# Optimization experiments

Hardware: AMD Instinct MI355X
Metric: run time of the kernel (lower is better)

The kernel has to match this reference:

```python
import jax, jax.numpy as jnp
import numpy as np

WD, WH, WW = 6, 6, 6
NUM_HEADS = 8
EPS = 1e-5


def setup_inputs() -> dict:
    key = jax.random.key(0)
    ks = jax.random.split(key, 4)
    B, C, D, H, W = 1, 128, 48, 48, 48
    return {
        "q_map": jax.random.normal(ks[0], (B, C, D, H, W), dtype=jnp.float32),
        "k_map": jax.random.normal(ks[1], (B, C, D, H, W), dtype=jnp.float32),
        "v_map": jax.random.normal(ks[2], (B, C, D, H, W), dtype=jnp.float32),
        "gamma_q": jnp.ones((C,), jnp.float32),
        "beta_q": jnp.zeros((C,), jnp.float32),
        "gamma_kv": jnp.ones((C,), jnp.float32),
        "beta_kv": jnp.zeros((C,), jnp.float32),
        "proj_w": jax.random.normal(ks[3], (C, C), dtype=jnp.float32) * (1.0 / np.sqrt(C)),
        "proj_b": jnp.zeros((C,), jnp.float32),
    }


def _layernorm(x, g, b):
    m = jnp.mean(x, axis=-1, keepdims=True)
    v = jnp.mean(jnp.square(x - m), axis=-1, keepdims=True)
    return (x - m) * jax.lax.rsqrt(v + EPS) * g + b


def _window_partition(x):
    # x: (B, D, H, W, C) -> windows: (B*nD*nH*nW, wd*wh*ww, C)
    B, D, H, W, C = x.shape
    pd, ph, pw = (WD - D % WD) % WD, (WH - H % WH) % WH, (WW - W % WW) % WW
    if pd or ph or pw:
        x = jnp.pad(x, ((0, 0), (0, pd), (0, ph), (0, pw), (0, 0)))
    Dp, Hp, Wp = D + pd, H + ph, W + pw
    x = x.reshape(B, Dp // WD, WD, Hp // WH, WH, Wp // WW, WW, C)
    x = jnp.transpose(x, (0, 1, 3, 5, 2, 4, 6, 7))
    return x.reshape(-1, WD * WH * WW, C), (D, H, W, Dp, Hp, Wp)


def _window_reverse(windows, meta):
    D, H, W, Dp, Hp, Wp = meta
    C = windows.shape[-1]
    nD, nH, nW = Dp // WD, Hp // WH, Wp // WW
    B = windows.shape[0] // (nD * nH * nW)
    x = windows.reshape(B, nD, nH, nW, WD, WH, WW, C)
    x = jnp.transpose(x, (0, 1, 4, 2, 5, 3, 6, 7)).reshape(B, Dp, Hp, Wp, C)
    return x[:, :D, :H, :W, :]


def reference(q_map, k_map, v_map, gamma_q, beta_q, gamma_kv, beta_kv, proj_w, proj_b):
    # (B, C, D, H, W) -> (B, D, H, W, C)
    q_map = jnp.transpose(q_map, (0, 2, 3, 4, 1))
    k_map = jnp.transpose(k_map, (0, 2, 3, 4, 1))
    v_map = jnp.transpose(v_map, (0, 2, 3, 4, 1))

    q, meta = _window_partition(q_map)
    k, _ = _window_partition(k_map)
    v, _ = _window_partition(v_map)

    q = _layernorm(q, gamma_q, beta_q)
    k = _layernorm(k, gamma_kv, beta_kv)
    v = _layernorm(v, gamma_kv, beta_kv)

    Bw, Nq, C = q.shape
    dh = C // NUM_HEADS
    q = q.reshape(Bw, Nq, NUM_HEADS, dh)
    k = k.reshape(Bw, -1, NUM_HEADS, dh)
    v = v.reshape(Bw, -1, NUM_HEADS, dh)

    scale = 1.0 / np.sqrt(dh).astype(np.float32)
    scores = jnp.einsum("bqhd,bkhd->bhqk", q, k) * scale  # (Bw, h, Nq, Nk)
    attn = jax.nn.softmax(scores, axis=-1)
    out = jnp.einsum("bhqk,bkhd->bqhd", attn, v).reshape(Bw, Nq, C)

    out = out @ proj_w.T + proj_b
    out = _window_reverse(out, meta)
    return jnp.transpose(out, (0, 4, 1, 2, 3))  # (B, C, D, H, W)
```

## Files before the change

kernel.cpp:

```cpp
#include <hip/hip_runtime.h>
#include <hip/hip_bf16.h>

typedef short s16x8 __attribute__((ext_vector_type(8)));
typedef float f32x2 __attribute__((ext_vector_type(2)));
typedef float f32x4 __attribute__((ext_vector_type(4)));
typedef float f32x16 __attribute__((ext_vector_type(16)));
typedef unsigned int u32;
typedef unsigned short u16;
typedef u32 u32x4v __attribute__((ext_vector_type(4)));

#define TOK 216
#define T1 448
#define T2 896
#define SP 110592
#define BUF0 0
#define VOFF 57344
#define WOFF 122880
#define GBOFF 155648
#define LDS_OLD 157696
#define LDS_NEW 155648
#define TENB 28311552ull
#define WSNEED (3ull*TENB + 32768ull)
#define QSCALE 0.360673760f

__device__ __forceinline__ u32 pack2(float a, float b) {
  u16 lo = __builtin_bit_cast(u16, __float2bfloat16(a));
  u16 hi = __builtin_bit_cast(u16, __float2bfloat16(b));
  return (u32)lo | ((u32)hi << 16);
}
__device__ __forceinline__ int swz(int row, int inner) {
  return inner ^ ((row & 7) << 4);
}
__device__ __forceinline__ void gload16(const void* g, void* l) {
  __builtin_amdgcn_global_load_lds(
      (const __attribute__((address_space(1))) void*)g,
      (__attribute__((address_space(3))) void*)l, 16, 0, 0);
}

__device__ __forceinline__ void ln_stats(const f32x2* xv, float& mA, float& rA,
                                         float& mB, float& rB) {
  float sA = 0.f, s2A = 0.f, sB = 0.f, s2B = 0.f;
#pragma unroll
  for (int c = 0; c < 32; ++c) {
    sA += xv[c].x; s2A += xv[c].x * xv[c].x;
    sB += xv[c].y; s2B += xv[c].y * xv[c].y;
  }
  sA += __shfl_xor(sA, 1); s2A += __shfl_xor(s2A, 1);
  sB += __shfl_xor(sB, 1); s2B += __shfl_xor(s2B, 1);
  sA += __shfl_xor(sA, 2); s2A += __shfl_xor(s2A, 2);
  sB += __shfl_xor(sB, 2); s2B += __shfl_xor(s2B, 2);
  mA = sA * (1.0f / 128.0f);
  rA = rsqrtf(s2A * (1.0f / 128.0f) - mA * mA + 1e-5f);
  mB = sB * (1.0f / 128.0f);
  rB = rsqrtf(s2B * (1.0f / 128.0f) - mB * mB + 1e-5f);
}

template<bool MASK>
__device__ __forceinline__ void attn_step(const char* smem, int h, int kt,
                                          s16x8 qfh, int lane,
                                          f32x16& acc, float& lsum) {
  const int half = lane >> 5;
  const int krow = kt * 32 + (lane & 31);
  s16x8 kf = *(const s16x8*)(smem + BUF0 + krow * 256 +
                             swz(krow, h * 32 + half * 16));
  __builtin_amdgcn_s_setprio(1);
  f32x16 st = __builtin_amdgcn_mfma_f32_32x32x16_bf16(kf, qfh, (f32x16){}, 0, 0, 0);
  __builtin_amdgcn_s_setprio(0);
  const int vrow = h * 16 + (lane & 15);
  s16x8 vf0 = *(const s16x8*)(smem + VOFF + vrow * 512 +
                              swz(vrow, kt * 64 + half * 16));
  s16x8 vf1 = *(const s16x8*)(smem + VOFF + vrow * 512 +
                              swz(vrow, kt * 64 + 32 + half * 16));
  const int NR = MASK ? 12 : 16;
  u32 A[8];
  float ts0 = 0.f, ts1 = 0.f;
#pragma unroll
  for (int i = 0; i < 8; ++i) {
    float p0 = (2 * i < NR) ? __builtin_amdgcn_exp2f(st[2 * i]) : 0.f;
    float p1 = (2 * i + 1 < NR) ? __builtin_amdgcn_exp2f(st[2 * i + 1]) : 0.f;
    if (i & 1) ts1 += p0 + p1; else ts0 += p0 + p1;
    A[i] = pack2(p0, p1);
  }
  lsum += ts0 + ts1;
  s16x8 pf0 = __builtin_bit_cast(s16x8, (u32x4v){A[0], A[1], A[2], A[3]});
  s16x8 pf1 = __builtin_bit_cast(s16x8, (u32x4v){A[4], A[5], A[6], A[7]});
  __builtin_amdgcn_s_setprio(1);
  acc = __builtin_amdgcn_mfma_f32_32x32x16_bf16(vf0, pf0, acc, 0, 0, 0);
  acc = __builtin_amdgcn_mfma_f32_32x32x16_bf16(vf1, pf1, acc, 0, 0, 0);
  __builtin_amdgcn_s_setprio(0);
}

extern "C" __global__ __launch_bounds__(256)
void lnpre_kernel(const float* __restrict__ qm, const float* __restrict__ km,
                  const float* __restrict__ vm,
                  const float* __restrict__ gq, const float* __restrict__ bq,
                  const float* __restrict__ gkv, const float* __restrict__ bkv,
                  const float* __restrict__ pw,
                  u16* __restrict__ qn, u16* __restrict__ kn,
                  u16* __restrict__ vn, u16* __restrict__ wbf) {
  const int tid = threadIdx.x;
  const int bid = blockIdx.x;
  if (bid >= 2304) {
#pragma unroll
    for (int k = 0; k < 32; ++k) {
      int idx = tid + 256 * k;
      f32x2 w2 = *(const f32x2*)(pw + idx * 2);
      ((u32*)wbf)[idx] = pack2(w2.x, w2.y);
    }
    return;
  }
  __shared__ float lf[6144];
  __shared__ float gb[512];
  const int d = bid / 48, h = bid - d * 48;
  const int dh = d * 2304 + h * 48;
  if (tid < 128) {
    gb[tid] = gq[tid]; gb[128 + tid] = bq[tid];
    gb[256 + tid] = gkv[tid]; gb[384 + tid] = bkv[tid];
  }
  const int w = tid >> 2, q = tid & 3;
#pragma unroll 1
  for (int t = 0; t < 3; ++t) {
    const float* src = t == 0 ? qm : (t == 1 ? km : vm);
    u16* dst = t == 0 ? qn : (t == 1 ? kn : vn);
    const float* g = (t == 0) ? gb : gb + 256;
    const float* b = (t == 0) ? gb + 128 : gb + 384;
    const float scale = (t == 0) ? QSCALE : 1.0f;
#pragma unroll
    for (int k = 0; k < 6; ++k) {
      int j = tid + 256 * k;
      int ch = j / 12, wq = j - ch * 12;
      *(f32x4*)(lf + ch * 48 + wq * 4) =
          *(const f32x4*)(src + (long)ch * SP + dh + wq * 4);
    }
    __syncthreads();
    if (tid < 192) {
      float s = 0.f, s2 = 0.f;
#pragma unroll
      for (int c = 0; c < 32; ++c) {
        float x = lf[(q + 4 * c) * 48 + w];
        s += x; s2 += x * x;
      }
      s += __shfl_xor(s, 1); s2 += __shfl_xor(s2, 1);
      s += __shfl_xor(s, 2); s2 += __shfl_xor(s2, 2);
      float m = s * (1.f / 128.f);
      float r = rsqrtf(s2 * (1.f / 128.f) - m * m + 1e-5f);
      u32x4v* op = (u32x4v*)(dst + (long)(dh + w) * 128 + 32 * q);
#pragma unroll
      for (int v4 = 0; v4 < 4; ++v4) {
        u32x4v pk;
#pragma unroll
        for (int e = 0; e < 4; ++e) {
          int ch = 32 * q + v4 * 8 + 2 * e;
          float y0 = ((lf[ch * 48 + w] - m) * r * g[ch] + b[ch]) * scale;
          float y1 = ((lf[(ch + 1) * 48 + w] - m) * r * g[ch + 1] + b[ch + 1]) * scale;
          pk[e] = pack2(y0, y1);
        }
        op[v4] = pk;
      }
    }
    __syncthreads();
  }
}

extern "C" __global__ __launch_bounds__(T2, 1)
void attn2_kernel(const u16* __restrict__ qn, const u16* __restrict__ kn,
                  const u16* __restrict__ vn, const u16* __restrict__ wbf,
                  const float* __restrict__ pb, float* __restrict__ out) {
  extern __shared__ __align__(16) char smem[];
  const int tid = threadIdx.x;
  const int lane = tid & 63;
  const int wv = tid >> 6;
  const int wq = wv % 7;
  const int hb = (wv / 7) * 4;
  const int bid = blockIdx.x;
  const int wid = ((bid & 7) << 6) | (bid >> 3);
  const int wd = wid >> 6, wh = (wid >> 3) & 7, ww = wid & 7;
  const int wd6 = wd * 6, wh6 = wh * 6, ww6 = ww * 6;
  const int boff = wd6 * 2304 + wh6 * 48 + ww6;

  for (int uu = wv; uu < 140; uu += 14) {
    const u16* s; char* d;
    if (uu < 54) {
      int u = uu, row = 4 * u + (lane >> 4);
      int tq = row / 6;
      int g = (wd6 + tq / 6) * 2304 + (wh6 + tq % 6) * 48 + ww6 + row % 6;
      s = qn + g * 128 + (((lane & 15) ^ (row & 7)) << 3);
      d = smem + BUF0 + u * 1024;
    } else if (uu < 108) {
      int u = uu - 54, row = 4 * u + (lane >> 4);
      int tq = row / 6;
      int g = (wd6 + tq / 6) * 2304 + (wh6 + tq % 6) * 48 + ww6 + row % 6;
      s = vn + g * 128 + ((lane & 15) << 3);
      d = smem + VOFF + u * 1024;
    } else {
      int u = uu - 108, row = 4 * u + (lane >> 4);
      s = wbf + row * 128 + (((lane & 15) ^ (row & 7)) << 3);
      d = smem + WOFF + u * 1024;
    }
    gload16(s, d);
  }
  __syncthreads();

  s16x8 qf[4];
  {
    int row = wq * 32 + (lane & 31);
    int ib = (lane >> 5) * 16;
#pragma unroll
    for (int j = 0; j < 4; ++j)
      qf[j] = *(const s16x8*)(smem + BUF0 + row * 256 +
                              swz(row, (hb + j) * 32 + ib));
  }
  __syncthreads();

  for (int uu = wv; uu < 54; uu += 14) {
    int row = 4 * uu + (lane >> 4);
    int tq = row / 6;
    int g = (wd6 + tq / 6) * 2304 + (wh6 + tq % 6) * 48 + ww6 + row % 6;
    gload16(kn + g * 128 + (((lane & 15) ^ (row & 7)) << 3),
            smem + BUF0 + uu * 1024);
  }
  u32 tr[16];
#pragma unroll
  for (int k = 0; k < 8; ++k) {
    int u = tid + 896 * k;
    if (u < 6912) {
      int t = (u >> 6) * 2, c2 = u & 63;
      tr[2 * k]     = *(const u32*)(smem + VOFF + t * 256 + c2 * 4);
      tr[2 * k + 1] = *(const u32*)(smem + VOFF + t * 256 + 256 + c2 * 4);
    }
  }
  __syncthreads();

#pragma unroll
  for (int k = 0; k < 8; ++k) {
    int u = tid + 896 * k;
    if (u < 6912) {
      int t = (u >> 6) * 2, c2 = u & 63;
      int st = (t & ~12) | ((t & 4) << 1) | ((t & 8) >> 1);
      int c = 2 * c2;
      u32 w0 = (tr[2 * k] & 0xFFFFu) | (tr[2 * k + 1] << 16);
      u32 w1 = (tr[2 * k] >> 16) | (tr[2 * k + 1] & 0xFFFF0000u);
      *(u32*)(smem + VOFF + c * 512 + ((st * 2) ^ ((c & 7) << 4))) = w0;
      *(u32*)(smem + VOFF + (c + 1) * 512 + ((st * 2) ^ (((c + 1) & 7) << 4))) = w1;
    }
  }
  if (tid < 128) {
    int x = (tid & 7) << 4;
    *(u32*)(smem + VOFF + tid * 512 + (424 ^ x)) = 0;
    *(u32*)(smem + VOFF + tid * 512 + (428 ^ x)) = 0;
    *(u32*)(smem + VOFF + tid * 512 + (440 ^ x)) = 0;
    *(u32*)(smem + VOFF + tid * 512 + (444 ^ x)) = 0;
  }
  __syncthreads();

  u32 oPk[4][4];
#pragma unroll
  for (int hp = 0; hp < 2; ++hp) {
    const int h0 = hb + 2 * hp, h1 = h0 + 1;
    f32x16 a0 = {}, a1 = {};
    float l0 = 0.f, l1 = 0.f;
#pragma unroll 2
    for (int kt = 0; kt < 6; ++kt) {
      attn_step<false>(smem, h0, kt, qf[2 * hp], lane, a0, l0);
      attn_step<false>(smem, h1, kt, qf[2 * hp + 1], lane, a1, l1);
    }
    attn_step<true>(smem, h0, 6, qf[2 * hp], lane, a0, l0);
    attn_step<true>(smem, h1, 6, qf[2 * hp + 1], lane, a1, l1);
    l0 += __shfl_xor(l0, 32);
    l1 += __shfl_xor(l1, 32);
    float i0 = 1.0f / l0, i1 = 1.0f / l1;
#pragma unroll
    for (int r = 0; r < 4; ++r) {
      oPk[2 * hp][r]     = pack2(a0[2 * r] * i0, a0[2 * r + 1] * i0);
      oPk[2 * hp + 1][r] = pack2(a1[2 * r] * i1, a1[2 * r + 1] * i1);
    }
  }
  __syncthreads();

  {
    const int tok = wq * 32 + (lane & 31);
    const int half = lane >> 5;
#pragma unroll
    for (int j = 0; j < 4; ++j) {
      int chb = (hb + j) * 32 + half * 8;
      *(u32*)(smem + BUF0 + tok * 256 + swz(tok, chb))      = oPk[j][0];
      *(u32*)(smem + BUF0 + tok * 256 + swz(tok, chb + 4))  = oPk[j][1];
      *(u32*)(smem + BUF0 + tok * 256 + swz(tok, chb + 16)) = oPk[j][2];
      *(u32*)(smem + BUF0 + tok * 256 + swz(tok, chb + 20)) = oPk[j][3];
    }
  }
  __syncthreads();

  {
    int tok = wv * 16 + (lane & 15);
    s16x8 bfr[4];
#pragma unroll
    for (int kk = 0; kk < 4; ++kk)
      bfr[kk] = *(const s16x8*)(smem + BUF0 + tok * 256 +
                                swz(tok, kk * 64 + (lane >> 4) * 16));
    bool tokValid = tok < TOK;
    int tdd = tok / 36, trr = tok - tdd * 36;
    int thh = trr / 6, tww = trr - thh * 6;
    int pos = boff + tdd * 2304 + thh * 48 + tww;
#pragma unroll 1
    for (int jt = 0; jt < 8; ++jt) {
      f32x4 acc = {};
#pragma unroll
      for (int kk = 0; kk < 4; ++kk) {
        int rw = jt * 16 + (lane & 15);
        s16x8 af = *(const s16x8*)(smem + WOFF + rw * 256 +
                                   swz(rw, kk * 64 + (lane >> 4) * 16));
        acc = __builtin_amdgcn_mfma_f32_16x16x32_bf16(af, bfr[kk], acc, 0, 0, 0);
      }
      f32x4 pbv = *(const f32x4*)(pb + jt * 16 + (lane >> 4) * 4);
      if (tokValid) {
#pragma unroll
        for (int r = 0; r < 4; ++r) {
          int j = jt * 16 + (lane >> 4) * 4 + r;
          out[j * SP + pos] = acc[r] + pbv[r];
        }
      }
    }
  }
}

extern "C" __global__ __launch_bounds__(T1, 2)
void ca3d_kernel(const float* __restrict__ qm, const float* __restrict__ km,
                 const float* __restrict__ vm,
                 const float* __restrict__ gq, const float* __restrict__ bq,
                 const float* __restrict__ gkv, const float* __restrict__ bkv,
                 const float* __restrict__ pw, const float* __restrict__ pb,
                 float* __restrict__ out) {
  extern __shared__ __align__(16) char smem[];
  const int tid = threadIdx.x;
  const int lane = tid & 63;
  const int wv = tid >> 6;
  const int bid = blockIdx.x;
  const int wid = ((bid & 7) << 6) | (bid >> 3);
  const int wd = wid >> 6, wh = (wid >> 3) & 7, ww = wid & 7;
  const int boff = wd * 6 * 2304 + wh * 6 * 48 + ww * 6;

  for (int i = tid * 16; i < VOFF + 65536; i += T1 * 16)
    *(f32x4*)(smem + i) = (f32x4){};
  if (tid < 128) {
    ((float*)(smem + GBOFF))[tid] = gq[tid];
    ((float*)(smem + GBOFF + 512))[tid] = bq[tid];
    ((float*)(smem + GBOFF + 1024))[tid] = gkv[tid];
    ((float*)(smem + GBOFF + 1536))[tid] = bkv[tid];
  }
  const bool lnAct = tid < 432;
  const int tp = tid >> 2;
  const int cbase = (tid & 3) * 32;
  const int tA = tp * 2, tB = tA + 1;
  int td = tA / 36, tr_ = tA - td * 36;
  int th_ = tr_ / 6, tw_ = tr_ - th_ * 6;
  const int gpos = boff + td * 2304 + th_ * 48 + tw_;
  const int vposA = (tA & ~0xC) | ((tA & 4) << 1) | ((tA & 8) >> 1);

  f32x2 qv[32], kv[32], vv[32];
  if (lnAct) {
#pragma unroll
    for (int c = 0; c < 32; ++c)
      qv[c] = *(const f32x2*)(qm + gpos + (cbase + c) * SP);
#pragma unroll
    for (int c = 0; c < 32; ++c)
      kv[c] = *(const f32x2*)(km + gpos + (cbase + c) * SP);
  }
  __syncthreads();
  const float* gql = (const float*)(smem + GBOFF);
  const float* bql = (const float*)(smem + GBOFF + 512);
  const float* gkl = (const float*)(smem + GBOFF + 1024);
  const float* bkl = (const float*)(smem + GBOFF + 1536);
  if (lnAct) {
    float mA, rA, mB, rB;
    ln_stats(qv, mA, rA, mB, rB);
#pragma unroll
    for (int c = 0; c < 32; c += 2) {
      int cc = cbase + c;
      float g0 = gql[cc], g1 = gql[cc + 1], b0 = bql[cc], b1 = bql[cc + 1];
      *(u32*)(smem + BUF0 + tA * 256 + swz(tA, cc * 2)) =
          pack2(((qv[c].x - mA) * rA * g0 + b0) * QSCALE,
                ((qv[c + 1].x - mA) * rA * g1 + b1) * QSCALE);
      *(u32*)(smem + BUF0 + tB * 256 + swz(tB, cc * 2)) =
          pack2(((qv[c].y - mB) * rB * g0 + b0) * QSCALE,
                ((qv[c + 1].y - mB) * rB * g1 + b1) * QSCALE);
    }
#pragma unroll
    for (int c = 0; c < 32; ++c)
      vv[c] = *(const f32x2*)(vm + gpos + (cbase + c) * SP);
  }
  __syncthreads();
  s16x8 qf[8];
  {
    int row = wv * 32 + (lane & 31);
    int ib = (lane >> 5) * 16;
#pragma unroll
    for (int h = 0; h < 8; ++h)
      qf[h] = *(const s16x8*)(smem + BUF0 + row * 256 + swz(row, h * 32 + ib));
  }
  __syncthreads();
  if (lnAct) {
    {
      float mA, rA, mB, rB;
      ln_stats(kv, mA, rA, mB, rB);
#pragma unroll
      for (int c = 0; c < 32; c += 2) {
        int cc = cbase + c;
        float g0 = gkl[cc], g1 = gkl[cc + 1], b0 = bkl[cc], b1 = bkl[cc + 1];
        *(u32*)(smem + BUF0 + tA * 256 + swz(tA, cc * 2)) =
            pack2((kv[c].x - mA) * rA * g0 + b0,
                  (kv[c + 1].x - mA) * rA * g1 + b1);
        *(u32*)(smem + BUF0 + tB * 256 + swz(tB, cc * 2)) =
            pack2((kv[c].y - mB) * rB * g0 + b0,
                  (kv[c + 1].y - mB) * rB * g1 + b1);
      }
    }
    {
      float mA, rA, mB, rB;
      ln_stats(vv, mA, rA, mB, rB);
#pragma unroll
      for (int c = 0; c < 32; ++c) {
        int cc = cbase + c;
        float g0 = gkl[cc], b0 = bkl[cc];
        *(u32*)(smem + VOFF + cc * 512 + swz(cc, vposA * 2)) =
            pack2((vv[c].x - mA) * rA * g0 + b0,
                  (vv[c].y - mB) * rB * g0 + b0);
      }
    }
  }
  for (int i = tid; i < 8192; i += T1) {
    int j = i >> 6, c2 = i & 63;
    f32x2 w2 = *(const f32x2*)(pw + j * 128 + c2 * 2);
    *(u32*)(smem + WOFF + j * 256 + swz(j, c2 * 4)) = pack2(w2.x, w2.y);
  }
  __syncthreads();
  u32 oPk[8][4];
#pragma unroll
  for (int hp = 0; hp < 4; ++hp) {
    const int h0 = hp * 2, h1 = h0 + 1;
    f32x16 a0 = {}, a1 = {};
    float l0 = 0.f, l1 = 0.f;
#pragma unroll 1
    for (int kt = 0; kt < 6; ++kt) {
      attn_step<false>(smem, h0, kt, qf[h0], lane, a0, l0);
      attn_step<false>(smem, h1, kt, qf[h1], lane, a1, l1);
    }
    attn_step<true>(smem, h0, 6, qf[h0], lane, a0, l0);
    attn_step<true>(smem, h1, 6, qf[h1], lane, a1, l1);
    l0 += __shfl_xor(l0, 32);
    l1 += __shfl_xor(l1, 32);
    float i0 = 1.0f / l0, i1 = 1.0f / l1;
#pragma unroll
    for (int r = 0; r < 4; ++r) {
      oPk[h0][r] = pack2(a0[2 * r] * i0, a0[2 * r + 1] * i0);
      oPk[h1][r] = pack2(a1[2 * r] * i1, a1[2 * r + 1] * i1);
    }
  }
  __syncthreads();
  {
    const int tok = wv * 32 + (lane & 31);
    const int half = lane >> 5;
#pragma unroll
    for (int h = 0; h < 8; ++h) {
      int chb = h * 32 + half * 8;
      *(u32*)(smem + BUF0 + tok * 256 + swz(tok, chb))      = oPk[h][0];
      *(u32*)(smem + BUF0 + tok * 256 + swz(tok, chb + 4))  = oPk[h][1];
      *(u32*)(smem + BUF0 + tok * 256 + swz(tok, chb + 16)) = oPk[h][2];
      *(u32*)(smem + BUF0 + tok * 256 + swz(tok, chb + 20)) = oPk[h][3];
    }
  }
  __syncthreads();
#pragma unroll 1
  for (int ti = 0; ti < 2; ++ti) {
    int tt = wv * 2 + ti;
    int tok = tt * 16 + (lane & 15);
    s16x8 bfr[4];
#pragma unroll
    for (int kk = 0; kk < 4; ++kk)
      bfr[kk] = *(const s16x8*)(smem + BUF0 + tok * 256 +
                                swz(tok, kk * 64 + (lane >> 4) * 16));
    bool tokValid = tok < TOK;
    int tdd = tok / 36, trr = tok - tdd * 36;
    int thh = trr / 6, tww = trr - thh * 6;
    int pos = boff + tdd * 2304 + thh * 48 + tww;
#pragma unroll 1
    for (int jt = 0; jt < 8; ++jt) {
      f32x4 acc = {};
#pragma unroll
      for (int kk = 0; kk < 4; ++kk) {
        int rw = jt * 16 + (lane & 15);
        s16x8 af = *(const s16x8*)(smem + WOFF + rw * 256 +
                                   swz(rw, kk * 64 + (lane >> 4) * 16));
        acc = __builtin_amdgcn_mfma_f32_16x16x32_bf16(af, bfr[kk], acc, 0, 0, 0);
      }
      f32x4 pbv = *(const f32x4*)(pb + jt * 16 + (lane >> 4) * 4);
      if (tokValid) {
#pragma unroll
        for (int r = 0; r < 4; ++r) {
          int j = jt * 16 + (lane >> 4) * 4 + r;
          out[j * SP + pos] = acc[r] + pbv[r];
        }
      }
    }
  }
}

extern "C" void kernel_launch(void* const* d_in, const int* in_sizes, int n_in,
                              void* d_out, int out_size, void* d_ws, size_t ws_size,
                              hipStream_t stream) {
  const float* qm  = (const float*)d_in[0];
  const float* km  = (const float*)d_in[1];
  const float* vm  = (const float*)d_in[2];
  const float* gq  = (const float*)d_in[3];
  const float* bq  = (const float*)d_in[4];
  const float* gkv = (const float*)d_in[5];
  const float* bkv = (const float*)d_in[6];
  const float* pw  = (const float*)d_in[7];
  const float* pb  = (const float*)d_in[8];
  if (ws_size >= WSNEED) {
    u16* qn  = (u16*)d_ws;
    u16* kn  = (u16*)((char*)d_ws + TENB);
    u16* vn  = (u16*)((char*)d_ws + 2 * TENB);
    u16* wbf = (u16*)((char*)d_ws + 3 * TENB);
    hipLaunchKernelGGL(lnpre_kernel, dim3(2305), dim3(256), 0, stream,
                       qm, km, vm, gq, bq, gkv, bkv, pw, qn, kn, vn, wbf);
    hipLaunchKernelGGL(attn2_kernel, dim3(512), dim3(T2), LDS_NEW, stream,
                       qn, kn, vn, wbf, pb, (float*)d_out);
  } else {
    hipLaunchKernelGGL(ca3d_kernel, dim3(512), dim3(T1), LDS_OLD, stream,
                       qm, km, vm, gq, bq, gkv, bkv, pw, pb, (float*)d_out);
  }
}
```

Measured before the change: 154.2 us.

## Pre-transpose V per window in prepass and slim attention kernel LDS footprint

The LayerNorm prepass now writes V already transposed per window (channel-major, padded to 224 tokens) and writes the projection weight pre-swizzled, so the attention kernel no longer stages V and W in LDS or transposes V in shared memory. The attention kernel drops from 896 threads with ~152KB LDS to 448 threads with ~57KB static LDS, holding only K. It reads Q, V and W fragments directly from global/L2 and processes one head at a time, aiming for multiple blocks per CU. The cost is more scattered global reads of V and W inside the inner loop, plus extra transpose work in the prepass.

```diff
diff --git a/kernel.cpp b/kernel.cpp
--- a/kernel.cpp
+++ b/kernel.cpp
@@ -7,20 +7,20 @@
 typedef float f32x16 __attribute__((ext_vector_type(16)));
 typedef unsigned int u32;
 typedef unsigned short u16;
+typedef u32 u32x2v __attribute__((ext_vector_type(2)));
 typedef u32 u32x4v __attribute__((ext_vector_type(4)));
 
 #define TOK 216
 #define T1 448
-#define T2 896
 #define SP 110592
 #define BUF0 0
 #define VOFF 57344
 #define WOFF 122880
 #define GBOFF 155648
 #define LDS_OLD 157696
-#define LDS_NEW 155648
 #define TENB 28311552ull
-#define WSNEED (3ull*TENB + 32768ull)
+#define VTB  29360128ull
+#define WSNEED (2ull*TENB + VTB + 32768ull)
 #define QSCALE 0.360673760f
 
 __device__ __forceinline__ u32 pack2(float a, float b) {
@@ -56,9 +56,45 @@
 }
 
 template<bool MASK>
-__device__ __forceinline__ void attn_step(const char* smem, int h, int kt,
-                                          s16x8 qfh, int lane,
-                                          f32x16& acc, float& lsum) {
+__device__ __forceinline__ void attn_stepD(const char* smem, const u16* __restrict__ vt,
+                                           int wid, int h, int kt, s16x8 qfh,
+                                           int lane, f32x16& acc, float& lsum) {
+  const int half = lane >> 5;
+  const int krow = kt * 32 + (lane & 31);
+  s16x8 kf = *(const s16x8*)(smem + krow * 256 + swz(krow, h * 32 + half * 16));
+  __builtin_amdgcn_s_setprio(1);
+  f32x16 st = __builtin_amdgcn_mfma_f32_32x32x16_bf16(kf, qfh, (f32x16){}, 0, 0, 0);
+  __builtin_amdgcn_s_setprio(0);
+  const u16* vb = vt + ((h * 16 + (lane & 15)) * 512 + wid) * 224 + kt * 32 + 4 * half;
+  u32x2v va0 = *(const u32x2v*)(vb);
+  u32x2v va1 = *(const u32x2v*)(vb + 8);
+  u32x2v va2 = *(const u32x2v*)(vb + 16);
+  u32x2v va3 = *(const u32x2v*)(vb + 24);
+  const int NR = MASK ? 12 : 16;
+  u32 A[8];
+  float ts0 = 0.f, ts1 = 0.f;
+#pragma unroll
+  for (int i = 0; i < 8; ++i) {
+    float p0 = (2 * i < NR) ? __builtin_amdgcn_exp2f(st[2 * i]) : 0.f;
+    float p1 = (2 * i + 1 < NR) ? __builtin_amdgcn_exp2f(st[2 * i + 1]) : 0.f;
+    if (i & 1) ts1 += p0 + p1; else ts0 += p0 + p1;
+    A[i] = pack2(p0, p1);
+  }
+  lsum += ts0 + ts1;
+  s16x8 pf0 = __builtin_bit_cast(s16x8, (u32x4v){A[0], A[1], A[2], A[3]});
+  s16x8 pf1 = __builtin_bit_cast(s16x8, (u32x4v){A[4], A[5], A[6], A[7]});
+  s16x8 vf0 = __builtin_bit_cast(s16x8, (u32x4v){va0[0], va0[1], va1[0], va1[1]});
+  s16x8 vf1 = __builtin_bit_cast(s16x8, (u32x4v){va2[0], va2[1], va3[0], va3[1]});
+  __builtin_amdgcn_s_setprio(1);
+  acc = __builtin_amdgcn_mfma_f32_32x32x16_bf16(vf0, pf0, acc, 0, 0, 0);
+  acc = __builtin_amdgcn_mfma_f32_32x32x16_bf16(vf1, pf1, acc, 0, 0, 0);
+  __builtin_amdgcn_s_setprio(0);
+}
+
+template<bool MASK>
+__device__ __forceinline__ void attn_stepF(const char* smem, int h, int kt,
+                                           s16x8 qfh, int lane,
+                                           f32x16& acc, float& lsum) {
   const int half = lane >> 5;
   const int krow = kt * 32 + (lane & 31);
   s16x8 kf = *(const s16x8*)(smem + BUF0 + krow * 256 +
@@ -97,22 +133,27 @@
                   const float* __restrict__ gkv, const float* __restrict__ bkv,
                   const float* __restrict__ pw,
                   u16* __restrict__ qn, u16* __restrict__ kn,
-                  u16* __restrict__ vn, u16* __restrict__ wbf) {
+                  u16* __restrict__ vt, u16* __restrict__ wsg) {
   const int tid = threadIdx.x;
   const int bid = blockIdx.x;
   if (bid >= 2304) {
 #pragma unroll
     for (int k = 0; k < 32; ++k) {
       int idx = tid + 256 * k;
-      f32x2 w2 = *(const f32x2*)(pw + idx * 2);
-      ((u32*)wbf)[idx] = pack2(w2.x, w2.y);
+      int j = idx >> 6, cu = idx & 63;
+      int c = 2 * cu;
+      int cs = (c & ~12) | ((c & 4) << 1) | ((c & 8) >> 1);
+      ((u32*)wsg)[idx] = pack2(pw[j * 128 + cs], pw[j * 128 + cs + 1]);
     }
     return;
   }
   __shared__ float lf[6144];
   __shared__ float gb[512];
+  __shared__ u32 vstage32[64 * 48];
   const int d = bid / 48, h = bid - d * 48;
   const int dh = d * 2304 + h * 48;
+  const int widbase = (d / 6) * 64 + (h / 6) * 8;
+  const int tokbase = (d % 6) * 36 + (h % 6) * 6;
   if (tid < 128) {
     gb[tid] = gq[tid]; gb[128 + tid] = bq[tid];
     gb[256 + tid] = gkv[tid]; gb[384 + tid] = bkv[tid];
@@ -121,7 +162,6 @@
 #pragma unroll 1
   for (int t = 0; t < 3; ++t) {
     const float* src = t == 0 ? qm : (t == 1 ? km : vm);
-    u16* dst = t == 0 ? qn : (t == 1 ? kn : vn);
     const float* g = (t == 0) ? gb : gb + 256;
     const float* b = (t == 0) ? gb + 128 : gb + 384;
     const float scale = (t == 0) ? QSCALE : 1.0f;
@@ -144,181 +184,122 @@
       s += __shfl_xor(s, 2); s2 += __shfl_xor(s2, 2);
       float m = s * (1.f / 128.f);
       float r = rsqrtf(s2 * (1.f / 128.f) - m * m + 1e-5f);
-      u32x4v* op = (u32x4v*)(dst + (long)(dh + w) * 128 + 32 * q);
-#pragma unroll
-      for (int v4 = 0; v4 < 4; ++v4) {
-        u32x4v pk;
-#pragma unroll
-        for (int e = 0; e < 4; ++e) {
-          int ch = 32 * q + v4 * 8 + 2 * e;
-          float y0 = ((lf[ch * 48 + w] - m) * r * g[ch] + b[ch]) * scale;
-          float y1 = ((lf[(ch + 1) * 48 + w] - m) * r * g[ch + 1] + b[ch + 1]) * scale;
-          pk[e] = pack2(y0, y1);
+      if (t < 2) {
+        u16* dst = (t == 0) ? qn : kn;
+        u32x4v* op = (u32x4v*)(dst + (long)(dh + w) * 128 + 32 * q);
+#pragma unroll
+        for (int v4 = 0; v4 < 4; ++v4) {
+          u32x4v pk;
+#pragma unroll
+          for (int e = 0; e < 4; ++e) {
+            int ch = 32 * q + v4 * 8 + 2 * e;
+            float y0 = ((lf[ch * 48 + w] - m) * r * g[ch] + b[ch]) * scale;
+            float y1 = ((lf[(ch + 1) * 48 + w] - m) * r * g[ch + 1] + b[ch + 1]) * scale;
+            pk[e] = pack2(y0, y1);
+          }
+          op[v4] = pk;
         }
-        op[v4] = pk;
+      } else {
+#pragma unroll
+        for (int cc2 = 0; cc2 < 16; ++cc2) {
+          int ch = 32 * q + 2 * cc2;
+          float y0 = (lf[ch * 48 + w] - m) * r * g[ch] + b[ch];
+          float y1 = (lf[(ch + 1) * 48 + w] - m) * r * g[ch + 1] + b[ch + 1];
+          vstage32[(16 * q + cc2) * 48 + w] = pack2(y0, y1);
+        }
       }
     }
     __syncthreads();
   }
-}
-
-extern "C" __global__ __launch_bounds__(T2, 1)
-void attn2_kernel(const u16* __restrict__ qn, const u16* __restrict__ kn,
-                  const u16* __restrict__ vn, const u16* __restrict__ wbf,
+  for (int i = tid; i < 3072; i += 256) {
+    int ch = i / 24, rem = i - ch * 24;
+    int w2 = rem / 3, t2 = rem - w2 * 3;
+    int wloc = w2 * 6 + t2 * 2;
+    u32 va = vstage32[(ch >> 1) * 48 + wloc];
+    u32 vb = vstage32[(ch >> 1) * 48 + wloc + 1];
+    u32 lo = (ch & 1) ? (va >> 16) : (va & 0xFFFFu);
+    u32 hi = (ch & 1) ? (vb >> 16) : (vb & 0xFFFFu);
+    *(u32*)(vt + (long)(ch * 512 + widbase + w2) * 224 + tokbase + 2 * t2) =
+        lo | (hi << 16);
+  }
+}
+
+extern "C" __global__ __launch_bounds__(T1, 4)
+void attn3_kernel(const u16* __restrict__ qn, const u16* __restrict__ kn,
+                  const u16* __restrict__ vt, const u16* __restrict__ wsg,
                   const float* __restrict__ pb, float* __restrict__ out) {
-  extern __shared__ __align__(16) char smem[];
-  const int tid = threadIdx.x;
-  const int lane = tid & 63;
-  const int wv = tid >> 6;
-  const int wq = wv % 7;
-  const int hb = (wv / 7) * 4;
+  __shared__ __align__(16) char smem[57344 + 512];
+  float* pbl = (float*)(smem + 57344);
+  const int tid = threadIdx.x, lane = tid & 63, wv = tid >> 6;
+  const int half = lane >> 5;
   const int bid = blockIdx.x;
   const int wid = ((bid & 7) << 6) | (bid >> 3);
-  const int wd = wid >> 6, wh = (wid >> 3) & 7, ww = wid & 7;
-  const int wd6 = wd * 6, wh6 = wh * 6, ww6 = ww * 6;
+  const int wd6 = (wid >> 6) * 6, wh6 = ((wid >> 3) & 7) * 6, ww6 = (wid & 7) * 6;
   const int boff = wd6 * 2304 + wh6 * 48 + ww6;
 
-  for (int uu = wv; uu < 140; uu += 14) {
-    const u16* s; char* d;
-    if (uu < 54) {
-      int u = uu, row = 4 * u + (lane >> 4);
-      int tq = row / 6;
-      int g = (wd6 + tq / 6) * 2304 + (wh6 + tq % 6) * 48 + ww6 + row % 6;
-      s = qn + g * 128 + (((lane & 15) ^ (row & 7)) << 3);
-      d = smem + BUF0 + u * 1024;
-    } else if (uu < 108) {
-      int u = uu - 54, row = 4 * u + (lane >> 4);
-      int tq = row / 6;
-      int g = (wd6 + tq / 6) * 2304 + (wh6 + tq % 6) * 48 + ww6 + row % 6;
-      s = vn + g * 128 + ((lane & 15) << 3);
-      d = smem + VOFF + u * 1024;
-    } else {
-      int u = uu - 108, row = 4 * u + (lane >> 4);
-      s = wbf + row * 128 + (((lane & 15) ^ (row & 7)) << 3);
-      d = smem + WOFF + u * 1024;
-    }
-    gload16(s, d);
-  }
-  __syncthreads();
-
-  s16x8 qf[4];
-  {
-    int row = wq * 32 + (lane & 31);
-    int ib = (lane >> 5) * 16;
-#pragma unroll
-    for (int j = 0; j < 4; ++j)
-      qf[j] = *(const s16x8*)(smem + BUF0 + row * 256 +
-                              swz(row, (hb + j) * 32 + ib));
-  }
-  __syncthreads();
-
-  for (int uu = wv; uu < 54; uu += 14) {
+  for (int uu = wv; uu < 54; uu += 7) {
     int row = 4 * uu + (lane >> 4);
     int tq = row / 6;
     int g = (wd6 + tq / 6) * 2304 + (wh6 + tq % 6) * 48 + ww6 + row % 6;
-    gload16(kn + g * 128 + (((lane & 15) ^ (row & 7)) << 3),
-            smem + BUF0 + uu * 1024);
-  }
-  u32 tr[16];
-#pragma unroll
-  for (int k = 0; k < 8; ++k) {
-    int u = tid + 896 * k;
-    if (u < 6912) {
-      int t = (u >> 6) * 2, c2 = u & 63;
-      tr[2 * k]     = *(const u32*)(smem + VOFF + t * 256 + c2 * 4);
-      tr[2 * k + 1] = *(const u32*)(smem + VOFF + t * 256 + 256 + c2 * 4);
-    }
-  }
-  __syncthreads();
-
-#pragma unroll
-  for (int k = 0; k < 8; ++k) {
-    int u = tid + 896 * k;
-    if (u < 6912) {
-      int t = (u >> 6) * 2, c2 = u & 63;
-      int st = (t & ~12) | ((t & 4) << 1) | ((t & 8) >> 1);
-      int c = 2 * c2;
-      u32 w0 = (tr[2 * k] & 0xFFFFu) | (tr[2 * k + 1] << 16);
-      u32 w1 = (tr[2 * k] >> 16) | (tr[2 * k + 1] & 0xFFFF0000u);
-      *(u32*)(smem + VOFF + c * 512 + ((st * 2) ^ ((c & 7) << 4))) = w0;
-      *(u32*)(smem + VOFF + (c + 1) * 512 + ((st * 2) ^ (((c + 1) & 7) << 4))) = w1;
-    }
-  }
-  if (tid < 128) {
-    int x = (tid & 7) << 4;
-    *(u32*)(smem + VOFF + tid * 512 + (424 ^ x)) = 0;
-    *(u32*)(smem + VOFF + tid * 512 + (428 ^ x)) = 0;
-    *(u32*)(smem + VOFF + tid * 512 + (440 ^ x)) = 0;
-    *(u32*)(smem + VOFF + tid * 512 + (444 ^ x)) = 0;
-  }
-  __syncthreads();
-
-  u32 oPk[4][4];
-#pragma unroll
-  for (int hp = 0; hp < 2; ++hp) {
-    const int h0 = hb + 2 * hp, h1 = h0 + 1;
-    f32x16 a0 = {}, a1 = {};
-    float l0 = 0.f, l1 = 0.f;
-#pragma unroll 2
-    for (int kt = 0; kt < 6; ++kt) {
-      attn_step<false>(smem, h0, kt, qf[2 * hp], lane, a0, l0);
-      attn_step<false>(smem, h1, kt, qf[2 * hp + 1], lane, a1, l1);
-    }
-    attn_step<true>(smem, h0, 6, qf[2 * hp], lane, a0, l0);
-    attn_step<true>(smem, h1, 6, qf[2 * hp + 1], lane, a1, l1);
-    l0 += __shfl_xor(l0, 32);
-    l1 += __shfl_xor(l1, 32);
-    float i0 = 1.0f / l0, i1 = 1.0f / l1;
-#pragma unroll
-    for (int r = 0; r < 4; ++r) {
-      oPk[2 * hp][r]     = pack2(a0[2 * r] * i0, a0[2 * r + 1] * i0);
-      oPk[2 * hp + 1][r] = pack2(a1[2 * r] * i1, a1[2 * r + 1] * i1);
-    }
-  }
-  __syncthreads();
-
+    gload16(kn + g * 128 + (((lane & 15) ^ (row & 7)) << 3), smem + uu * 1024);
+  }
+  if (tid < 128) pbl[tid] = pb[tid];
+
+  int qrow = wv * 32 + (lane & 31);
+  if (qrow > 215) qrow = 215;
+  int qg;
   {
-    const int tok = wq * 32 + (lane & 31);
-    const int half = lane >> 5;
-#pragma unroll
-    for (int j = 0; j < 4; ++j) {
-      int chb = (hb + j) * 32 + half * 8;
-      *(u32*)(smem + BUF0 + tok * 256 + swz(tok, chb))      = oPk[j][0];
-      *(u32*)(smem + BUF0 + tok * 256 + swz(tok, chb + 4))  = oPk[j][1];
-      *(u32*)(smem + BUF0 + tok * 256 + swz(tok, chb + 16)) = oPk[j][2];
-      *(u32*)(smem + BUF0 + tok * 256 + swz(tok, chb + 20)) = oPk[j][3];
-    }
-  }
-  __syncthreads();
-
-  {
-    int tok = wv * 16 + (lane & 15);
-    s16x8 bfr[4];
-#pragma unroll
-    for (int kk = 0; kk < 4; ++kk)
-      bfr[kk] = *(const s16x8*)(smem + BUF0 + tok * 256 +
-                                swz(tok, kk * 64 + (lane >> 4) * 16));
-    bool tokValid = tok < TOK;
+    int tq = qrow / 6;
+    qg = (wd6 + tq / 6) * 2304 + (wh6 + tq % 6) * 48 + ww6 + qrow % 6;
+  }
+  s16x8 qf[8];
+#pragma unroll
+  for (int h = 0; h < 8; ++h)
+    qf[h] = *(const s16x8*)(qn + qg * 128 + h * 16 + half * 8);
+  __syncthreads();
+
+  u32 oPk[8][4];
+#pragma unroll 1
+  for (int h = 0; h < 8; ++h) {
+    f32x16 a = {};
+    float l = 0.f;
+#pragma unroll 1
+    for (int kt = 0; kt < 6; ++kt)
+      attn_stepD<false>(smem, vt, wid, h, kt, qf[h], lane, a, l);
+    attn_stepD<true>(smem, vt, wid, h, 6, qf[h], lane, a, l);
+    l += __shfl_xor(l, 32);
+    float li = 1.0f / l;
+#pragma unroll
+    for (int r = 0; r < 4; ++r)
+      oPk[h][r] = pack2(a[2 * r] * li, a[2 * r + 1] * li);
+  }
+
+  const int tok = wv * 32 + (lane & 31);
+  const bool valid = tok < TOK;
+  int pos = 0;
+  if (valid) {
     int tdd = tok / 36, trr = tok - tdd * 36;
     int thh = trr / 6, tww = trr - thh * 6;
-    int pos = boff + tdd * 2304 + thh * 48 + tww;
-#pragma unroll 1
-    for (int jt = 0; jt < 8; ++jt) {
-      f32x4 acc = {};
-#pragma unroll
-      for (int kk = 0; kk < 4; ++kk) {
-        int rw = jt * 16 + (lane & 15);
-        s16x8 af = *(const s16x8*)(smem + WOFF + rw * 256 +
-                                   swz(rw, kk * 64 + (lane >> 4) * 16));
-        acc = __builtin_amdgcn_mfma_f32_16x16x32_bf16(af, bfr[kk], acc, 0, 0, 0);
-      }
-      f32x4 pbv = *(const f32x4*)(pb + jt * 16 + (lane >> 4) * 4);
-      if (tokValid) {
-#pragma unroll
-        for (int r = 0; r < 4; ++r) {
-          int j = jt * 16 + (lane >> 4) * 4 + r;
-          out[j * SP + pos] = acc[r] + pbv[r];
-        }
+    pos = boff + tdd * 2304 + thh * 48 + tww;
+  }
+#pragma unroll 1
+  for (int js = 0; js < 4; ++js) {
+    f32x16 acc = {};
+#pragma unroll
+    for (int hs = 0; hs < 8; ++hs) {
+      s16x8 af = *(const s16x8*)(wsg + (js * 32 + (lane & 31)) * 128 +
+                                 hs * 16 + half * 8);
+      s16x8 bo = __builtin_bit_cast(s16x8,
+          (u32x4v){oPk[hs][0], oPk[hs][1], oPk[hs][2], oPk[hs][3]});
+      __builtin_amdgcn_s_setprio(1);
+      acc = __builtin_amdgcn_mfma_f32_32x32x16_bf16(af, bo, acc, 0, 0, 0);
+      __builtin_amdgcn_s_setprio(0);
+    }
+    if (valid) {
+#pragma unroll
+      for (int r = 0; r < 16; ++r) {
+        int j = js * 32 + (r & 3) + 8 * (r >> 2) + 4 * half;
+        out[j * SP + pos] = acc[r] + pbl[j];
       }
     }
   }
@@ -442,11 +423,11 @@
     float l0 = 0.f, l1 = 0.f;
 #pragma unroll 1
     for (int kt = 0; kt < 6; ++kt) {
-      attn_step<false>(smem, h0, kt, qf[h0], lane, a0, l0);
-      attn_step<false>(smem, h1, kt, qf[h1], lane, a1, l1);
-    }
-    attn_step<true>(smem, h0, 6, qf[h0], lane, a0, l0);
-    attn_step<true>(smem, h1, 6, qf[h1], lane, a1, l1);
+      attn_stepF<false>(smem, h0, kt, qf[h0], lane, a0, l0);
+      attn_stepF<false>(smem, h1, kt, qf[h1], lane, a1, l1);
+    }
+    attn_stepF<true>(smem, h0, 6, qf[h0], lane, a0, l0);
+    attn_stepF<true>(smem, h1, 6, qf[h1], lane, a1, l1);
     l0 += __shfl_xor(l0, 32);
     l1 += __shfl_xor(l1, 32);
     float i0 = 1.0f / l0, i1 = 1.0f / l1;
@@ -520,12 +501,12 @@
   if (ws_size >= WSNEED) {
     u16* qn  = (u16*)d_ws;
     u16* kn  = (u16*)((char*)d_ws + TENB);
-    u16* vn  = (u16*)((char*)d_ws + 2 * TENB);
-    u16* wbf = (u16*)((char*)d_ws + 3 * TENB);
+    u16* vt  = (u16*)((char*)d_ws + 2 * TENB);
+    u16* wsg = (u16*)((char*)d_ws + 2 * TENB + VTB);
     hipLaunchKernelGGL(lnpre_kernel, dim3(2305), dim3(256), 0, stream,
-                       qm, km, vm, gq, bq, gkv, bkv, pw, qn, kn, vn, wbf);
-    hipLaunchKernelGGL(attn2_kernel, dim3(512), dim3(T2), LDS_NEW, stream,
-                       qn, kn, vn, wbf, pb, (float*)d_out);
+                       qm, km, vm, gq, bq, gkv, bkv, pw, qn, kn, vt, wsg);
+    hipLaunchKernelGGL(attn3_kernel, dim3(512), dim3(T1), 0, stream,
+                       qn, kn, vt, wsg, pb, (float*)d_out);
   } else {
     hipLaunchKernelGGL(ca3d_kernel, dim3(512), dim3(T1), LDS_OLD, stream,
                        qm, km, vm, gq, bq, gkv, bkv, pw, pb, (float*)d_out);
```

Result: slower. 231.8 us (+50.3%).
